# Kernel tuning notes

Hardware: AMD Instinct MI355X
Metric: run time of the kernel (lower is better)

## Reference

```python
import jax, jax.numpy as jnp
import numpy as np

FSAMPLE = 100.0


def _butter_sos(N, Wn, btype):
    """Butterworth digital SOS design (bilinear transform), matching scipy.signal.butter
    up to section ordering (same transfer function)."""
    fs = 2.0
    k = np.arange(1, N + 1)
    p = np.exp(1j * np.pi * (2 * k + N - 1) / (2 * N))  # analog prototype poles, gain 1
    if btype == 'low':
        warped = 2 * fs * np.tan(np.pi * float(Wn) / fs)
        p = p * warped
        z = np.array([], dtype=complex)
        gain = warped ** N
    else:  # bandpass
        w1 = 2 * fs * np.tan(np.pi * Wn[0] / fs)
        w2 = 2 * fs * np.tan(np.pi * Wn[1] / fs)
        bw = w2 - w1
        wo = np.sqrt(w1 * w2)
        plp = p * bw / 2.0
        disc = np.sqrt(plp ** 2 - wo ** 2)
        p = np.concatenate([plp + disc, plp - disc])
        z = np.zeros(N, dtype=complex)
        gain = bw ** N
    fs2 = 2 * fs
    gain = gain * np.real(np.prod(fs2 - z) / np.prod(fs2 - p))
    pd = (fs2 + p) / (fs2 - p)            # bilinear-transformed poles
    # digital zeros: mapped analog zeros plus padding zeros at z=-1
    # lowpass -> all zeros at -1 -> b = [1,2,1]; bandpass -> zeros at +1 and -1 -> b = [1,0,-1]
    b_proto = np.array([1.0, 2.0, 1.0]) if btype == 'low' else np.array([1.0, 0.0, -1.0])
    pp = pd[np.imag(pd) > 0]              # one pole per conjugate pair
    rows = []
    for i, pi in enumerate(pp):
        a = np.array([1.0, -2.0 * np.real(pi), np.abs(pi) ** 2])
        b = b_proto * (gain if i == 0 else 1.0)
        rows.append(np.concatenate([b, a]))
    return np.stack(rows).astype(np.float32)  # [n_sections, 6]


def _biquad(w, b, a):
    """Direct-form I biquad along time. w: [NC, T]; b, a: length-3 (a[0] may != 1)."""
    b = b / a[0]
    a = a / a[0]

    def step(carry, xn):  # xn: [NC]
        x1, x2, y1, y2 = carry
        y = b[0] * xn + b[1] * x1 + b[2] * x2 - a[1] * y1 - a[2] * y2
        return (xn, x1, y, y1), y

    z = jnp.zeros_like(w[:, 0])
    _, ys = jax.lax.scan(step, (z, z, z, z), w.T)  # ys: [T, NC]
    return ys.T


def _sosfilt(w, sos):
    for i in range(sos.shape[0]):  # small fixed number of sections
        w = _biquad(w, sos[i, :3], sos[i, 3:])
    return w


def setup_inputs() -> dict:
    key = jax.random.key(0)
    B, T, C = 16, 16384, 64
    x = jax.random.normal(key, (B, T, C), dtype=jnp.float32)
    nyq = FSAMPLE / 2.0
    bp_sos = jnp.asarray(_butter_sos(2, [6.0 / nyq, 20.0 / nyq], 'band'))
    lp_sos = jnp.asarray(_butter_sos(4, 10.0 / nyq, 'low'))
    return {"x": x, "bp_sos": bp_sos, "lp_sos": lp_sos}


def reference(x, bp_sos, lp_sos):
    B, T, C = x.shape
    w = jnp.transpose(x, (0, 2, 1)).reshape(B * C, T)  # filter along time
    w = _sosfilt(w, bp_sos)          # bandpass 6-20 Hz
    w = _sosfilt(w * w, lp_sos)      # square then lowpass 10 Hz
    return jnp.transpose(w.reshape(B, C, T), (0, 2, 1))
```

## Files before the change

### kernel.cpp

```cpp
#include <hip/hip_runtime.h>

#define B_LEN 16
#define T_LEN 16384
#define C_LEN 64
#define CHUNK 128
#define WARM  64

__global__ __launch_bounds__(256, 2) void iir_pipe_kernel(
    const float* __restrict__ x,
    const float* __restrict__ bp,
    const float* __restrict__ lp,
    float* __restrict__ out)
{
    const int c     = threadIdx.x & 63;
    const int bsub  = threadIdx.x >> 6;
    const int b     = blockIdx.y * 4 + bsub;
    const int chunk = blockIdx.x;

    const float b10 = bp[0], b11 = bp[1], b12 = bp[2],  a11 = -bp[4],  a12 = -bp[5];
    const float b20 = bp[6], b21 = bp[7], b22 = bp[8],  a21 = -bp[10], a22 = -bp[11];
    const float b30 = lp[0], b31 = lp[1], b32 = lp[2],  a31 = -lp[4],  a32 = -lp[5];
    const float b40 = lp[6], b41 = lp[7], b42 = lp[8],  a41 = -lp[10], a42 = -lp[11];

    const int t_out0 = chunk * CHUNK;
    const int warm   = (t_out0 < WARM) ? t_out0 : WARM;
    const int t0     = t_out0 - warm;

    float s11 = 0.f, s12 = 0.f;
    float s21 = 0.f, s22 = 0.f;
    float s31 = 0.f, s32 = 0.f;
    float s41 = 0.f, s42 = 0.f;

    const float* __restrict__ lq = x   + ((size_t)b * T_LEN + t0)     * C_LEN + c;
    float*       __restrict__ po = out + ((size_t)b * T_LEN + t_out0) * C_LEN + c;

    auto step = [&](float xn) -> float {
        float y1 = fmaf(b10, xn, s11);
        s11 = fmaf(b11, xn, fmaf(a11, y1, s12));
        s12 = fmaf(b12, xn, a12 * y1);
        float y2 = fmaf(b20, y1, s21);
        s21 = fmaf(b21, y1, fmaf(a21, y2, s22));
        s22 = fmaf(b22, y1, a22 * y2);
        float v = y2 * y2;
        float y3 = fmaf(b30, v, s31);
        s31 = fmaf(b31, v, fmaf(a31, y3, s32));
        s32 = fmaf(b32, v, a32 * y3);
        float y4 = fmaf(b40, y3, s41);
        s41 = fmaf(b41, y3, fmaf(a41, y4, s42));
        s42 = fmaf(b42, y3, a42 * y4);
        return y4;
    };

    float P0[8], P1[8], P2[8], P3[8];

    auto load8 = [&](float* d) {
#pragma unroll
        for (int j = 0; j < 8; ++j) d[j] = lq[j * C_LEN];
        lq += 8 * C_LEN;
    };
    auto warm8 = [&](const float* d) {
#pragma unroll
        for (int j = 0; j < 8; ++j) step(d[j]);
    };
    auto emit8 = [&](const float* d) {
        float y[8];
#pragma unroll
        for (int j = 0; j < 8; ++j) y[j] = step(d[j]);
#pragma unroll
        for (int j = 0; j < 8; ++j)
            __builtin_nontemporal_store(y[j], po + j * C_LEN);
        po += 8 * C_LEN;
    };
    auto fence = [&]() { __builtin_amdgcn_sched_barrier(0); };

    load8(P0); load8(P1); load8(P2); load8(P3);
    fence();

    const int nrot = warm >> 5;
    for (int r = 0; r < nrot; ++r) {
        warm8(P0); load8(P0); fence();
        warm8(P1); load8(P1); fence();
        warm8(P2); load8(P2); fence();
        warm8(P3); load8(P3); fence();
    }
#pragma unroll 1
    for (int r = 0; r < (CHUNK - 32) / 32; ++r) {
        emit8(P0); load8(P0); fence();
        emit8(P1); load8(P1); fence();
        emit8(P2); load8(P2); fence();
        emit8(P3); load8(P3); fence();
    }
    emit8(P0); fence();
    emit8(P1); fence();
    emit8(P2); fence();
    emit8(P3);
}

extern "C" void kernel_launch(void* const* d_in, const int* in_sizes, int n_in,
                              void* d_out, int out_size, void* d_ws, size_t ws_size,
                              hipStream_t stream) {
    const float* x  = (const float*)d_in[0];
    const float* bp = (const float*)d_in[1];
    const float* lp = (const float*)d_in[2];
    float* out      = (float*)d_out;

    dim3 grid(T_LEN / CHUNK, B_LEN / 4);
    dim3 block(256);
    iir_pipe_kernel<<<grid, block, 0, stream>>>(x, bp, lp, out);
}
```

Before: 117.2 us.

## Halve chunk size, raise occupancy, and batch output stores per 32 samples

Time chunks shrink from 128 to 64 samples, which doubles the grid, and the launch bounds ask for 4 blocks per CU instead of 2. Outputs are kept in a 32-element register buffer and written in bursts instead of after every 8 steps, so stores no longer sit inside the serial recurrence. The tradeoff is that each chunk still spends 64 warm-up samples, so redundant work rises from half the useful work to equal to it, and the extra registers may limit occupancy.

```diff
diff --git a/kernel.cpp b/kernel.cpp
--- a/kernel.cpp
+++ b/kernel.cpp
@@ -3,10 +3,10 @@
 #define B_LEN 16
 #define T_LEN 16384
 #define C_LEN 64
-#define CHUNK 128
+#define CHUNK 64
 #define WARM  64
 
-__global__ __launch_bounds__(256, 2) void iir_pipe_kernel(
+__global__ __launch_bounds__(256, 4) void iir_defer_kernel(
     const float* __restrict__ x,
     const float* __restrict__ bp,
     const float* __restrict__ lp,
@@ -52,6 +52,7 @@
     };
 
     float P0[8], P1[8], P2[8], P3[8];
+    float Y[32];
 
     auto load8 = [&](float* d) {
 #pragma unroll
@@ -62,14 +63,9 @@
 #pragma unroll
         for (int j = 0; j < 8; ++j) step(d[j]);
     };
-    auto emit8 = [&](const float* d) {
-        float y[8];
+    auto emit8 = [&](const float* d, float* y) {
 #pragma unroll
         for (int j = 0; j < 8; ++j) y[j] = step(d[j]);
-#pragma unroll
-        for (int j = 0; j < 8; ++j)
-            __builtin_nontemporal_store(y[j], po + j * C_LEN);
-        po += 8 * C_LEN;
     };
     auto fence = [&]() { __builtin_amdgcn_sched_barrier(0); };
 
@@ -77,23 +73,32 @@
     fence();
 
     const int nrot = warm >> 5;
+#pragma unroll 1
     for (int r = 0; r < nrot; ++r) {
         warm8(P0); load8(P0); fence();
         warm8(P1); load8(P1); fence();
         warm8(P2); load8(P2); fence();
         warm8(P3); load8(P3); fence();
     }
-#pragma unroll 1
-    for (int r = 0; r < (CHUNK - 32) / 32; ++r) {
-        emit8(P0); load8(P0); fence();
-        emit8(P1); load8(P1); fence();
-        emit8(P2); load8(P2); fence();
-        emit8(P3); load8(P3); fence();
-    }
-    emit8(P0); fence();
-    emit8(P1); fence();
-    emit8(P2); fence();
-    emit8(P3);
+
+    emit8(P0, Y +  0); load8(P0); fence();
+    emit8(P1, Y +  8); load8(P1); fence();
+    emit8(P2, Y + 16); load8(P2); fence();
+    emit8(P3, Y + 24); load8(P3); fence();
+
+#pragma unroll
+    for (int i = 0; i < 32; ++i)
+        __builtin_nontemporal_store(Y[i], po + i * C_LEN);
+    fence();
+
+    emit8(P0, Y +  0); fence();
+    emit8(P1, Y +  8); fence();
+    emit8(P2, Y + 16); fence();
+    emit8(P3, Y + 24); fence();
+
+#pragma unroll
+    for (int i = 0; i < 32; ++i)
+        __builtin_nontemporal_store(Y[i], po + (32 + i) * C_LEN);
 }
 
 extern "C" void kernel_launch(void* const* d_in, const int* in_sizes, int n_in,
@@ -106,5 +111,5 @@
 
     dim3 grid(T_LEN / CHUNK, B_LEN / 4);
     dim3 block(256);
-    iir_pipe_kernel<<<grid, block, 0, stream>>>(x, bp, lp, out);
+    iir_defer_kernel<<<grid, block, 0, stream>>>(x, bp, lp, out);
 }
```

Measured after the change: 120.4 us. +2.7%, slower.
